# Kernel optimization log

Measured on AMD Instinct MI355X. Metric: run time of the kernel, lower is better.

Reference implementation:

```python
import jax, jax.numpy as jnp
import numpy as np

HEAD = 8
DIM_IN = 512
PAD = (4, 4)            # pad = head - dim % head = 8 -> (4, 4)
DIM = DIM_IN + sum(PAD) # 520
DH = DIM // HEAD        # 65


def setup_inputs() -> dict:
    key = jax.random.key(0)
    k1, k2, k3, k4 = jax.random.split(key, 4)
    B, L = 4, 2048
    inp = jax.random.normal(k1, (B, L, DIM_IN), dtype=jnp.float32)
    # nn.Linear weights, shape (out, in), bias=False
    scale = 1.0 / np.sqrt(DIM)
    w_q = jax.random.uniform(k2, (DIM, DIM), jnp.float32, -scale, scale)
    w_k = jax.random.uniform(k3, (DIM, DIM), jnp.float32, -scale, scale)
    w_v = jax.random.uniform(k4, (DIM, DIM), jnp.float32, -scale, scale)
    return {"inp": inp, "w_q": w_q, "w_k": w_k, "w_v": w_v}


def reference(inp, w_q, w_k, w_v):
    # F.pad(inp, pad) pads the last (feature) dim
    x = jnp.pad(inp, ((0, 0), (0, 0), (PAD[0], PAD[1])))
    B, L, D = x.shape
    # project then split heads: [B, H, L, dh]
    def proj(w):
        return (x @ w.T).reshape(B, L, HEAD, DH).transpose(0, 2, 1, 3)
    q, k, v = proj(w_q), proj(w_k), proj(w_v)
    score = jnp.einsum('bhqd,bhkd->bhqk', q, k) / jnp.sqrt(jnp.float32(DH))
    attn = jax.nn.softmax(score, axis=-1)          # [B, H, L, L]
    # dropout is identity in eval/reference mode
    out = jnp.einsum('bhqk,bhkd->bhqd', attn, v)
    out = out.transpose(0, 2, 1, 3).reshape(B, L, D)
    out = out[:, :, PAD[0]:-PAD[1]]                # strip feature padding
    return out, attn
```

## Files before the change

kernel.cpp:

```cpp
#include <hip/hip_runtime.h>

typedef unsigned short u16;
typedef __bf16 bf16x8 __attribute__((ext_vector_type(8)));
typedef float f32x16 __attribute__((ext_vector_type(16)));
typedef unsigned short ushort8 __attribute__((ext_vector_type(8)));

#define QSCALE2 0.17894429680154087f

__device__ __forceinline__ u16 f2bf(float f) {
  unsigned u = __float_as_uint(f);
  u = (u + 0x7fffu + ((u >> 16) & 1u)) >> 16;
  return (u16)u;
}

__device__ __forceinline__ f32x16 zero16() {
  f32x16 z;
#pragma unroll
  for (int i = 0; i < 16; ++i) z[i] = 0.0f;
  return z;
}

__device__ __forceinline__ void gload_lds16(const u16* g, u16* l) {
  __builtin_amdgcn_global_load_lds(
      (const __attribute__((address_space(1))) void*)g,
      (__attribute__((address_space(3))) void*)l, 16, 0, 0);
}

__global__ __launch_bounds__(256) void cvt_x_kernel(const float4* __restrict__ in,
                                                    ushort4* __restrict__ out) {
  int i = blockIdx.x * 256 + threadIdx.x;
  float4 v = in[i];
  ushort4 o;
  o.x = f2bf(v.x); o.y = f2bf(v.y); o.z = f2bf(v.z); o.w = f2bf(v.w);
  out[i] = o;
}

__global__ __launch_bounds__(256) void cvt_w_kernel(const float* __restrict__ wq,
                                                    const float* __restrict__ wk,
                                                    const float* __restrict__ wv,
                                                    u16* __restrict__ wtt) {
  int id = blockIdx.x * 256 + threadIdx.x;
  int wsel = id / (544 * 512);
  int rem = id - wsel * (544 * 512);
  int j = rem >> 9, k = rem & 511;
  const float* wp = (wsel == 0) ? wq : (wsel == 1) ? wk : wv;
  float v = (j < 520) ? wp[j * 520 + k + 4] : 0.0f;
  wtt[id] = f2bf(v);
}

__global__ __launch_bounds__(256) void zero_kernel(uint4* __restrict__ p, int n) {
  int i = blockIdx.x * 256 + threadIdx.x;
  uint4 z = make_uint4(0u, 0u, 0u, 0u);
  for (; i < n; i += gridDim.x * 256) p[i] = z;
}

__global__ __launch_bounds__(256) void proj_kernel(const u16* __restrict__ xb,
                                                   const u16* __restrict__ wtt,
                                                   u16* __restrict__ qb,
                                                   u16* __restrict__ kpl,
                                                   u16* __restrict__ vpl) {
  int tid = threadIdx.x;
  int w = tid >> 6, l = tid & 63, lr = l & 31, lh = l >> 5;
  int m0 = blockIdx.y * 128 + w * 32;
  int g = blockIdx.x;

  const u16* ap = xb + (size_t)(m0 + lr) * 512 + lh * 8;

  f32x16 acc[4];
  const u16* bp[4];
  bool valid[4];
#pragma unroll
  for (int i = 0; i < 4; ++i) {
    int nt = g * 4 + i;
    valid[i] = (nt < 51);
    int ntc = valid[i] ? nt : 50;
    bp[i] = wtt + ((size_t)((ntc / 17) * 544 + (ntc % 17) * 32) + lr) * 512 + lh * 8;
    acc[i] = zero16();
  }

#pragma unroll 4
  for (int s = 0; s < 32; ++s) {
    bf16x8 a = *reinterpret_cast<const bf16x8*>(ap + s * 16);
#pragma unroll
    for (int i = 0; i < 4; ++i) {
      if (valid[i]) {
        bf16x8 b = *reinterpret_cast<const bf16x8*>(bp[i] + s * 16);
        acc[i] = __builtin_amdgcn_mfma_f32_32x32x16_bf16(a, b, acc[i], 0, 0, 0);
      }
    }
  }

#pragma unroll
  for (int i = 0; i < 4; ++i) {
    int nt = g * 4 + i;
    if (nt < 51) {
      int wsel = nt / 17;
      int j = (nt % 17) * 32 + lr;
      if (j < 520) {
        int h = j / 65, dh = j - h * 65;
        if (wsel == 2) {
#pragma unroll
          for (int g2 = 0; g2 < 4; ++g2) {
            int m = m0 + g2 * 8 + 4 * lh;
            int bb = m >> 11, lrow = m & 2047;
            int bh = bb * 8 + h;
            int kc = lrow >> 3;
            ushort4 vv;
            vv.x = f2bf(acc[i][4 * g2]);
            vv.y = f2bf(acc[i][4 * g2 + 1]);
            vv.z = f2bf(acc[i][4 * g2 + 2]);
            vv.w = f2bf(acc[i][4 * g2 + 3]);
            *reinterpret_cast<ushort4*>(
                &vpl[(((size_t)bh * 256 + kc) * 80 + dh) * 8 + 4 * lh]) = vv;
          }
        } else {
#pragma unroll
          for (int r = 0; r < 16; ++r) {
            int m = m0 + (r & 3) + 8 * (r >> 2) + 4 * lh;
            int bb = m >> 11, lrow = m & 2047;
            int bh = bb * 8 + h;
            if (wsel == 0) {
              qb[((size_t)bh * 2048 + lrow) * 80 + dh] = f2bf(acc[i][r] * QSCALE2);
            } else {
              kpl[(((size_t)bh * 10 + (dh >> 3)) * 2048 + lrow) * 8 + (dh & 7)] = f2bf(acc[i][r]);
            }
          }
        }
      }
    }
  }
}

__global__ __launch_bounds__(256, 2) void attn_kernel(const u16* __restrict__ qb,
                                                      const u16* __restrict__ kpl,
                                                      const u16* __restrict__ vpl,
                                                      float* __restrict__ out,
                                                      float* __restrict__ attn) {
  __shared__ u16 kvbuf[2][10240];
  __shared__ u16 plds[4][32][40];

  int b = blockIdx.x;
  int bh = (b & 7) + 8 * (b >> 7);
  int qblk = (b >> 3) & 15;
  int tid = threadIdx.x;
  int w = tid >> 6, l = tid & 63, lr = l & 31, lh = l >> 5;
  int q0 = qblk * 128 + w * 32;
  int phase = (b * 11) & 31;

  const u16* kbh = kpl + (size_t)bh * 163840;
  const u16* vbh = vpl + (size_t)bh * 163840;

  const u16* qptr = qb + ((size_t)bh * 2048 + q0 + lr) * 80 + lh * 8;
  bf16x8 qf[5];
#pragma unroll
  for (int s = 0; s < 5; ++s) qf[s] = *reinterpret_cast<const bf16x8*>(qptr + s * 16);

  float sum[16];
#pragma unroll
  for (int r2 = 0; r2 < 16; ++r2) sum[r2] = 0.0f;

#define STAGE_K128(kt, bufi)                                                  \
  {                                                                           \
    _Pragma("unroll")                                                         \
    for (int i = 0; i < 5; ++i) {                                             \
      int idx = w + i * 4;                                                    \
      int c = idx >> 1, half = idx & 1;                                       \
      gload_lds16(kbh + (size_t)c * 16384 + (kt) * 1024 + half * 512 + l * 8, \
                  &kvbuf[bufi][idx * 512]);                                   \
    }                                                                         \
  }

  STAGE_K128(0, 0);
  __syncthreads();
  int buf = 0;
  for (int t = 0; t < 16; ++t) {
    if (t < 15) STAGE_K128(t + 1, buf ^ 1);
#pragma unroll
    for (int sub = 0; sub < 4; ++sub) {
      f32x16 acc = zero16();
#pragma unroll
      for (int s = 0; s < 5; ++s) {
        bf16x8 bk = *reinterpret_cast<const bf16x8*>(
            &kvbuf[buf][((2 * s + lh) * 128 + sub * 32 + lr) * 8]);
        acc = __builtin_amdgcn_mfma_f32_32x32x16_bf16(qf[s], bk, acc, 0, 0, 0);
      }
#pragma unroll
      for (int r2 = 0; r2 < 16; ++r2)
        sum[r2] += __builtin_amdgcn_exp2f(acc[r2]);
    }
    __syncthreads();
    buf ^= 1;
  }

#pragma unroll
  for (int r2 = 0; r2 < 16; ++r2) {
    float s = sum[r2];
#pragma unroll
    for (int d = 1; d < 32; d <<= 1) s += __shfl_xor(s, d);
    sum[r2] = 1.0f / s;
  }

#define STAGE_KV64(t64, bufi)                                                 \
  {                                                                           \
    _Pragma("unroll")                                                         \
    for (int i = 0; i < 5; ++i) {                                             \
      int idx = w + i * 4;                                                    \
      const u16* src = (idx < 10)                                             \
          ? kbh + (size_t)idx * 16384 + (t64) * 512 + l * 8                   \
          : vbh + (size_t)(t64) * 5120 + (idx - 10) * 512 + l * 8;            \
      gload_lds16(src, &kvbuf[bufi][idx * 512]);                              \
    }                                                                         \
  }

  f32x16 O[3];
#pragma unroll
  for (int n = 0; n < 3; ++n) O[n] = zero16();

  float* attn_base = attn + ((size_t)bh * 2048 + q0) * 2048;

  STAGE_KV64(phase, 0);
  __syncthreads();
  buf = 0;
  for (int t = 0; t < 32; ++t) {
    int tt = (t + phase) & 31;
    if (t < 31) STAGE_KV64((tt + 1) & 31, buf ^ 1);
#pragma unroll
    for (int sub = 0; sub < 2; ++sub) {
      int key0 = tt * 64 + sub * 32;
      f32x16 acc = zero16();
#pragma unroll
      for (int s = 0; s < 5; ++s) {
        bf16x8 bk = *reinterpret_cast<const bf16x8*>(
            &kvbuf[buf][((2 * s + lh) * 64 + sub * 32 + lr) * 8]);
        acc = __builtin_amdgcn_mfma_f32_32x32x16_bf16(qf[s], bk, acc, 0, 0, 0);
      }
#pragma unroll
      for (int r2 = 0; r2 < 16; ++r2) {
        int row = (r2 & 3) + 8 * (r2 >> 2) + 4 * lh;
        float p = __builtin_amdgcn_exp2f(acc[r2]) * sum[r2];
        __builtin_nontemporal_store(p, &attn_base[(size_t)row * 2048 + key0 + lr]);
        plds[w][row][lr] = f2bf(p);
      }
#pragma unroll
      for (int ks = 0; ks < 2; ++ks) {
        bf16x8 pa = *reinterpret_cast<const bf16x8*>(&plds[w][lr][ks * 16 + lh * 8]);
#pragma unroll
        for (int n = 0; n < 3; ++n) {
          bf16x8 bv = *reinterpret_cast<const bf16x8*>(
              &kvbuf[buf][5120 + ((sub * 4 + 2 * ks + lh) * 80 + n * 32 + lr) * 8]);
          O[n] = __builtin_amdgcn_mfma_f32_32x32x16_bf16(pa, bv, O[n], 0, 0, 0);
        }
      }
    }
    asm volatile("s_waitcnt vmcnt(32)" ::: "memory");
    __builtin_amdgcn_s_barrier();
    buf ^= 1;
  }

  int bb = bh >> 3, h = bh & 7;
#pragma unroll
  for (int n = 0; n < 3; ++n) {
    int d = n * 32 + lr;
    int cc = h * 65 + d - 4;
    if (d < 65 && cc >= 0 && cc < 512) {
#pragma unroll
      for (int r2 = 0; r2 < 16; ++r2) {
        int row = (r2 & 3) + 8 * (r2 >> 2) + 4 * lh;
        out[((size_t)bb * 2048 + q0 + row) * 512 + cc] = O[n][r2];
      }
    }
  }
}

extern "C" void kernel_launch(void* const* d_in, const int* in_sizes, int n_in,
                              void* d_out, int out_size, void* d_ws, size_t ws_size,
                              hipStream_t stream) {
  (void)in_sizes; (void)n_in; (void)out_size; (void)ws_size;
  const float* inp = (const float*)d_in[0];
  const float* wq  = (const float*)d_in[1];
  const float* wk  = (const float*)d_in[2];
  const float* wv  = (const float*)d_in[3];

  char* ws = (char*)d_ws;
  u16* xb  = (u16*)(ws + 0);
  u16* wtt = (u16*)(ws + 8388608);
  u16* qb  = (u16*)(ws + 10059776);
  u16* kpl = (u16*)(ws + 20545536);
  u16* vpl = (u16*)(ws + 31031296);

  float* out  = (float*)d_out;
  float* attn = out + (size_t)4 * 2048 * 512;

  cvt_x_kernel<<<4096, 256, 0, stream>>>((const float4*)inp, (ushort4*)xb);
  cvt_w_kernel<<<3264, 256, 0, stream>>>(wq, wk, wv, wtt);
  zero_kernel<<<640, 256, 0, stream>>>((uint4*)qb, 655360);
  proj_kernel<<<dim3(13, 64), 256, 0, stream>>>(xb, wtt, qb, kpl, vpl);
  attn_kernel<<<512, 256, 0, stream>>>(qb, kpl, vpl, out, attn);
}
```

Baseline: 242.8 us.

## Process two 32-row query tiles per wave to halve K/V staging traffic

Each attention block now covers 256 query rows instead of 128, with each wave holding two query tiles. Every K/V tile staged into LDS is reused by both tiles, so K/V global loads per query are halved. The grid shrinks from 512 to 256 blocks, which on a 256-CU part means one block per CU and fewer waves in flight. The occupancy hint of 2 is dropped and register use roughly doubles for the accumulators and Q fragments, and the vmcnt wait is raised to match the larger number of outstanding stores.

```diff
diff --git a/kernel.cpp b/kernel.cpp
--- a/kernel.cpp
+++ b/kernel.cpp
@@ -131,33 +131,40 @@
   }
 }
 
-__global__ __launch_bounds__(256, 2) void attn_kernel(const u16* __restrict__ qb,
-                                                      const u16* __restrict__ kpl,
-                                                      const u16* __restrict__ vpl,
-                                                      float* __restrict__ out,
-                                                      float* __restrict__ attn) {
+__global__ __launch_bounds__(256) void attn_kernel(const u16* __restrict__ qb,
+                                                   const u16* __restrict__ kpl,
+                                                   const u16* __restrict__ vpl,
+                                                   float* __restrict__ out,
+                                                   float* __restrict__ attn) {
   __shared__ u16 kvbuf[2][10240];
   __shared__ u16 plds[4][32][40];
 
   int b = blockIdx.x;
-  int bh = (b & 7) + 8 * (b >> 7);
-  int qblk = (b >> 3) & 15;
+  int bh = (b & 7) + 8 * (b >> 6);
+  int qblk = (b >> 3) & 7;
   int tid = threadIdx.x;
   int w = tid >> 6, l = tid & 63, lr = l & 31, lh = l >> 5;
-  int q0 = qblk * 128 + w * 32;
+  int q0 = qblk * 256;
+  int qA = q0 + w * 32, qB = q0 + 128 + w * 32;
   int phase = (b * 11) & 31;
 
   const u16* kbh = kpl + (size_t)bh * 163840;
   const u16* vbh = vpl + (size_t)bh * 163840;
 
-  const u16* qptr = qb + ((size_t)bh * 2048 + q0 + lr) * 80 + lh * 8;
-  bf16x8 qf[5];
-#pragma unroll
-  for (int s = 0; s < 5; ++s) qf[s] = *reinterpret_cast<const bf16x8*>(qptr + s * 16);
-
-  float sum[16];
-#pragma unroll
-  for (int r2 = 0; r2 < 16; ++r2) sum[r2] = 0.0f;
+  bf16x8 qf[2][5];
+#pragma unroll
+  for (int qt = 0; qt < 2; ++qt) {
+    const u16* qptr = qb + ((size_t)bh * 2048 + (qt ? qB : qA) + lr) * 80 + lh * 8;
+#pragma unroll
+    for (int s = 0; s < 5; ++s)
+      qf[qt][s] = *reinterpret_cast<const bf16x8*>(qptr + s * 16);
+  }
+
+  float sum[2][16];
+#pragma unroll
+  for (int qt = 0; qt < 2; ++qt)
+#pragma unroll
+    for (int r2 = 0; r2 < 16; ++r2) sum[qt][r2] = 0.0f;
 
 #define STAGE_K128(kt, bufi)                                                  \
   {                                                                           \
@@ -177,28 +184,33 @@
     if (t < 15) STAGE_K128(t + 1, buf ^ 1);
 #pragma unroll
     for (int sub = 0; sub < 4; ++sub) {
-      f32x16 acc = zero16();
-#pragma unroll
-      for (int s = 0; s < 5; ++s) {
-        bf16x8 bk = *reinterpret_cast<const bf16x8*>(
-            &kvbuf[buf][((2 * s + lh) * 128 + sub * 32 + lr) * 8]);
-        acc = __builtin_amdgcn_mfma_f32_32x32x16_bf16(qf[s], bk, acc, 0, 0, 0);
-      }
-#pragma unroll
-      for (int r2 = 0; r2 < 16; ++r2)
-        sum[r2] += __builtin_amdgcn_exp2f(acc[r2]);
+#pragma unroll
+      for (int qt = 0; qt < 2; ++qt) {
+        f32x16 acc = zero16();
+#pragma unroll
+        for (int s = 0; s < 5; ++s) {
+          bf16x8 bk = *reinterpret_cast<const bf16x8*>(
+              &kvbuf[buf][((2 * s + lh) * 128 + sub * 32 + lr) * 8]);
+          acc = __builtin_amdgcn_mfma_f32_32x32x16_bf16(qf[qt][s], bk, acc, 0, 0, 0);
+        }
+#pragma unroll
+        for (int r2 = 0; r2 < 16; ++r2)
+          sum[qt][r2] += __builtin_amdgcn_exp2f(acc[r2]);
+      }
     }
     __syncthreads();
     buf ^= 1;
   }
 
 #pragma unroll
-  for (int r2 = 0; r2 < 16; ++r2) {
-    float s = sum[r2];
-#pragma unroll
-    for (int d = 1; d < 32; d <<= 1) s += __shfl_xor(s, d);
-    sum[r2] = 1.0f / s;
-  }
+  for (int qt = 0; qt < 2; ++qt)
+#pragma unroll
+    for (int r2 = 0; r2 < 16; ++r2) {
+      float s = sum[qt][r2];
+#pragma unroll
+      for (int d = 1; d < 32; d <<= 1) s += __shfl_xor(s, d);
+      sum[qt][r2] = 1.0f / s;
+    }
 
 #define STAGE_KV64(t64, bufi)                                                 \
   {                                                                           \
@@ -212,11 +224,11 @@
     }                                                                         \
   }
 
-  f32x16 O[3];
-#pragma unroll
-  for (int n = 0; n < 3; ++n) O[n] = zero16();
-
-  float* attn_base = attn + ((size_t)bh * 2048 + q0) * 2048;
+  f32x16 O[2][3];
+#pragma unroll
+  for (int qt = 0; qt < 2; ++qt)
+#pragma unroll
+    for (int n = 0; n < 3; ++n) O[qt][n] = zero16();
 
   STAGE_KV64(phase, 0);
   __syncthreads();
@@ -227,46 +239,54 @@
 #pragma unroll
     for (int sub = 0; sub < 2; ++sub) {
       int key0 = tt * 64 + sub * 32;
-      f32x16 acc = zero16();
-#pragma unroll
-      for (int s = 0; s < 5; ++s) {
-        bf16x8 bk = *reinterpret_cast<const bf16x8*>(
-            &kvbuf[buf][((2 * s + lh) * 64 + sub * 32 + lr) * 8]);
-        acc = __builtin_amdgcn_mfma_f32_32x32x16_bf16(qf[s], bk, acc, 0, 0, 0);
-      }
-#pragma unroll
-      for (int r2 = 0; r2 < 16; ++r2) {
-        int row = (r2 & 3) + 8 * (r2 >> 2) + 4 * lh;
-        float p = __builtin_amdgcn_exp2f(acc[r2]) * sum[r2];
-        __builtin_nontemporal_store(p, &attn_base[(size_t)row * 2048 + key0 + lr]);
-        plds[w][row][lr] = f2bf(p);
-      }
-#pragma unroll
-      for (int ks = 0; ks < 2; ++ks) {
-        bf16x8 pa = *reinterpret_cast<const bf16x8*>(&plds[w][lr][ks * 16 + lh * 8]);
-#pragma unroll
-        for (int n = 0; n < 3; ++n) {
-          bf16x8 bv = *reinterpret_cast<const bf16x8*>(
-              &kvbuf[buf][5120 + ((sub * 4 + 2 * ks + lh) * 80 + n * 32 + lr) * 8]);
-          O[n] = __builtin_amdgcn_mfma_f32_32x32x16_bf16(pa, bv, O[n], 0, 0, 0);
-        }
-      }
-    }
-    asm volatile("s_waitcnt vmcnt(32)" ::: "memory");
+#pragma unroll
+      for (int qt = 0; qt < 2; ++qt) {
+        float* attn_base = attn + ((size_t)bh * 2048 + (qt ? qB : qA)) * 2048;
+        f32x16 acc = zero16();
+#pragma unroll
+        for (int s = 0; s < 5; ++s) {
+          bf16x8 bk = *reinterpret_cast<const bf16x8*>(
+              &kvbuf[buf][((2 * s + lh) * 64 + sub * 32 + lr) * 8]);
+          acc = __builtin_amdgcn_mfma_f32_32x32x16_bf16(qf[qt][s], bk, acc, 0, 0, 0);
+        }
+#pragma unroll
+        for (int r2 = 0; r2 < 16; ++r2) {
+          int row = (r2 & 3) + 8 * (r2 >> 2) + 4 * lh;
+          float p = __builtin_amdgcn_exp2f(acc[r2]) * sum[qt][r2];
+          __builtin_nontemporal_store(p, &attn_base[(size_t)row * 2048 + key0 + lr]);
+          plds[w][row][lr] = f2bf(p);
+        }
+#pragma unroll
+        for (int ks = 0; ks < 2; ++ks) {
+          bf16x8 pa = *reinterpret_cast<const bf16x8*>(&plds[w][lr][ks * 16 + lh * 8]);
+#pragma unroll
+          for (int n = 0; n < 3; ++n) {
+            bf16x8 bv = *reinterpret_cast<const bf16x8*>(
+                &kvbuf[buf][5120 + ((sub * 4 + 2 * ks + lh) * 80 + n * 32 + lr) * 8]);
+            O[qt][n] = __builtin_amdgcn_mfma_f32_32x32x16_bf16(pa, bv, O[qt][n], 0, 0, 0);
+          }
+        }
+      }
+    }
+    asm volatile("s_waitcnt vmcnt(48)" ::: "memory");
     __builtin_amdgcn_s_barrier();
     buf ^= 1;
   }
 
   int bb = bh >> 3, h = bh & 7;
 #pragma unroll
-  for (int n = 0; n < 3; ++n) {
-    int d = n * 32 + lr;
-    int cc = h * 65 + d - 4;
-    if (d < 65 && cc >= 0 && cc < 512) {
-#pragma unroll
-      for (int r2 = 0; r2 < 16; ++r2) {
-        int row = (r2 & 3) + 8 * (r2 >> 2) + 4 * lh;
-        out[((size_t)bb * 2048 + q0 + row) * 512 + cc] = O[n][r2];
+  for (int qt = 0; qt < 2; ++qt) {
+    int qx = qt ? qB : qA;
+#pragma unroll
+    for (int n = 0; n < 3; ++n) {
+      int d = n * 32 + lr;
+      int cc = h * 65 + d - 4;
+      if (d < 65 && cc >= 0 && cc < 512) {
+#pragma unroll
+        for (int r2 = 0; r2 < 16; ++r2) {
+          int row = (r2 & 3) + 8 * (r2 >> 2) + 4 * lh;
+          out[((size_t)bb * 2048 + qx + row) * 512 + cc] = O[qt][n][r2];
+        }
       }
     }
   }
@@ -295,5 +315,5 @@
   cvt_w_kernel<<<3264, 256, 0, stream>>>(wq, wk, wv, wtt);
   zero_kernel<<<640, 256, 0, stream>>>((uint4*)qb, 655360);
   proj_kernel<<<dim3(13, 64), 256, 0, stream>>>(xb, wtt, qb, kpl, vpl);
-  attn_kernel<<<512, 256, 0, stream>>>(qb, kpl, vpl, out, attn);
-}
+  attn_kernel<<<256, 256, 0, stream>>>(qb, kpl, vpl, out, attn);
+}
```

New measurement: 256.9 us. +5.8%, slower.
